# Kernel optimization log

Hardware: AMD Instinct MI355X
Metric: run time of the kernel (lower is better)

## Reference

```python
import jax, jax.numpy as jnp
import numpy as np

TOP_K = 2


def layer_norm(x, g, b, eps=1e-5):
    m = jnp.mean(x, axis=-1, keepdims=True)
    v = jnp.mean((x - m) ** 2, axis=-1, keepdims=True)
    return (x - m) * jax.lax.rsqrt(v + eps) * g + b


def setup_inputs() -> dict:
    key = jax.random.key(0)
    ks = jax.random.split(key, 6)
    B, P, D, E, K = 8, 1024, 1024, 8, TOP_K
    x = jax.random.normal(ks[0], (B, P, D), dtype=jnp.float32)
    noise = jax.random.normal(ks[1], (B * P * K, D), dtype=jnp.float32) * 1e-5
    Wg = jax.random.normal(ks[2], (D, E), dtype=jnp.float32) * 0.02
    bg = jnp.zeros((E,), dtype=jnp.float32)
    W1 = jax.random.normal(ks[3], (E, D, D), dtype=jnp.float32) * 0.02
    b1 = jnp.zeros((E, D), dtype=jnp.float32)
    W2 = jax.random.normal(ks[4], (E, D, D), dtype=jnp.float32) * 0.02
    b2 = jnp.zeros((E, D), dtype=jnp.float32)
    ln_g = jnp.ones((E, D), dtype=jnp.float32)
    ln_b = jnp.zeros((E, D), dtype=jnp.float32)
    gn_g = jnp.ones((D,), dtype=jnp.float32)
    gn_b = jnp.zeros((D,), dtype=jnp.float32)
    return {"x": x, "noise": noise, "Wg": Wg, "bg": bg, "W1": W1, "b1": b1,
            "W2": W2, "b2": b2, "ln_g": ln_g, "ln_b": ln_b, "gn_g": gn_g, "gn_b": gn_b}


def reference(x, noise, Wg, bg, W1, b1, W2, b2, ln_g, ln_b, gn_g, gn_b):
    # Eval-mode forward of Allocator (aux_loss == 0, not returned).
    B, P, D = x.shape
    E = Wg.shape[1]
    K = TOP_K
    N = B * P
    logits = jnp.einsum('bpd,de->bpe', x, Wg) + bg          # [B,P,E]
    probs = jax.nn.softmax(logits, axis=-1).reshape(N, E)
    _topk_probs, topk_idx = jax.lax.top_k(probs, K)          # probs unused in eval combine
    flat_idx = topk_idx.reshape(-1)                          # [N*K]
    sample_idx = jnp.repeat(jnp.arange(N), K)                # [N*K]
    batch_idx = sample_idx // P                              # [N*K]
    xg = x.reshape(N, D)[sample_idx] + noise                 # [N*K, D] gathered token copies
    sums = []
    for e in range(E):  # fixed small expert loop
        h = jax.nn.gelu(xg @ W1[e] + b1[e], approximate=False)
        y = h @ W2[e] + b2[e] + xg                           # Mlp + residual
        y = layer_norm(y, ln_g[e], ln_b[e])                  # Expert.norm
        m = (flat_idx == e)[:, None]
        # one_hot(batch_idx).T @ masked_output == per-batch segment sum (unweighted)
        sums.append(jax.ops.segment_sum(jnp.where(m, y, 0.0), batch_idx, num_segments=B))
    out = jnp.stack(sums, axis=0).transpose(1, 0, 2)         # [B, E, D]
    return layer_norm(out, gn_g, gn_b)
```

## Files before the change

kernel.cpp:

```cpp
#include <hip/hip_runtime.h>
#include <hip/hip_bf16.h>
#include <math.h>

#define D 1024
#define NTOK 8192
#define NSLOT 16384
#define NGRP 64
#define MAXTILE 136

typedef short bf16x8 __attribute__((ext_vector_type(8)));
typedef float floatx4 __attribute__((ext_vector_type(4)));

__device__ __forceinline__ unsigned short f2bf(float f) {
    __hip_bfloat16 h = __float2bfloat16(f);
    return *reinterpret_cast<unsigned short*>(&h);
}
__device__ __forceinline__ float bf2f(unsigned short u) {
    unsigned int v = ((unsigned int)u) << 16;
    return __uint_as_float(v);
}

__device__ __forceinline__ void load_lds16(const void* g, void* l) {
    __builtin_amdgcn_global_load_lds(
        (const __attribute__((address_space(1))) unsigned int*)g,
        (__attribute__((address_space(3))) unsigned int*)l, 16, 0, 0);
}

__global__ void zero_kernel(int* __restrict__ grp_cnt, float* __restrict__ S) {
    int i = blockIdx.x * 256 + threadIdx.x;
    if (i < NGRP) grp_cnt[i] = 0;
    if (i < 64 * D) S[i] = 0.f;
}

__global__ void route_kernel(const float* __restrict__ x, const float* __restrict__ Wg,
                             const float* __restrict__ bg, int* __restrict__ slot_e,
                             int* __restrict__ grp_cnt) {
    int wave = threadIdx.x >> 6;
    int lane = threadIdx.x & 63;
    int tok = blockIdx.x * 4 + wave;
    const float* xr = x + (size_t)tok * D;
    float acc[8] = {0.f,0.f,0.f,0.f,0.f,0.f,0.f,0.f};
    for (int k = lane; k < D; k += 64) {
        float xv = xr[k];
        const float4* w4 = reinterpret_cast<const float4*>(Wg + k * 8);
        float4 a = w4[0], b = w4[1];
        acc[0] += xv * a.x; acc[1] += xv * a.y; acc[2] += xv * a.z; acc[3] += xv * a.w;
        acc[4] += xv * b.x; acc[5] += xv * b.y; acc[6] += xv * b.z; acc[7] += xv * b.w;
    }
#pragma unroll
    for (int e = 0; e < 8; e++) {
#pragma unroll
        for (int off = 32; off > 0; off >>= 1)
            acc[e] += __shfl_xor(acc[e], off, 64);
    }
    if (lane == 0) {
        float lg[8];
#pragma unroll
        for (int e = 0; e < 8; e++) lg[e] = acc[e] + bg[e];
        int e1 = 0; float b1v = lg[0];
#pragma unroll
        for (int e = 1; e < 8; e++) if (lg[e] > b1v) { b1v = lg[e]; e1 = e; }
        int e2 = -1; float b2v = -3.0e38f;
#pragma unroll
        for (int e = 0; e < 8; e++) { if (e == e1) continue; if (lg[e] > b2v) { b2v = lg[e]; e2 = e; } }
        int b = tok >> 10;
        slot_e[2 * tok] = e1;
        slot_e[2 * tok + 1] = e2;
        atomicAdd(&grp_cnt[e1 * 8 + b], 1);
        atomicAdd(&grp_cnt[e2 * 8 + b], 1);
    }
}

__global__ void prefix_kernel(const int* __restrict__ grp_cnt, int* __restrict__ goff,
                              int* __restrict__ cursor, int2* __restrict__ tile_tab) {
    if (threadIdx.x != 0) return;
    int s = 0;
    for (int g = 0; g < NGRP; g++) { goff[g] = s; cursor[g] = s; s += grp_cnt[g]; }
    goff[NGRP] = s;
    int t = 0;
    for (int e = 0; e < 8; e++) {
        int cnt = goff[e * 8 + 8] - goff[e * 8];
        for (int m0 = 0; m0 < cnt; m0 += 128) tile_tab[t++] = make_int2(e, m0);
    }
    for (; t < MAXTILE; t++) tile_tab[t] = make_int2(-1, 0);
}

__global__ void build_xg_kernel(const float* __restrict__ x, const float* __restrict__ noise,
                                const int* __restrict__ slot_e, int* __restrict__ cursor,
                                unsigned short* __restrict__ xg) {
    int wave = threadIdx.x >> 6;
    int lane = threadIdx.x & 63;
    int slot = blockIdx.x * 4 + wave;
    int e = slot_e[slot];
    int b = slot >> 11;
    int row = 0;
    if (lane == 0) row = atomicAdd(&cursor[e * 8 + b], 1);
    row = __shfl(row, 0, 64);
    int tok = slot >> 1;
    const float4* xr = reinterpret_cast<const float4*>(x + (size_t)tok * D);
    const float4* nr = reinterpret_cast<const float4*>(noise + (size_t)slot * D);
    ushort4* og = reinterpret_cast<ushort4*>(xg + (size_t)row * D);
    for (int i = lane; i < D / 4; i += 64) {
        float4 a = xr[i], n = nr[i];
        ushort4 o;
        o.x = f2bf(a.x + n.x); o.y = f2bf(a.y + n.y);
        o.z = f2bf(a.z + n.z); o.w = f2bf(a.w + n.w);
        og[i] = o;
    }
}

__global__ void wconv_kernel(const float* __restrict__ W1, const float* __restrict__ W2,
                             unsigned short* __restrict__ W1t, unsigned short* __restrict__ W2t) {
    int z = blockIdx.y;
    int mat = z & 1, e = z >> 1;
    int kb = blockIdx.x;
    const float* src = (mat ? W2 : W1) + (size_t)e * D * D + (size_t)kb * 8 * D;
    unsigned short* dst = (mat ? W2t : W1t) + (size_t)e * D * D + (size_t)kb * (D * 8);
    int t = threadIdx.x;
    float4 v[8];
#pragma unroll
    for (int k = 0; k < 8; k++)
        v[k] = reinterpret_cast<const float4*>(src + (size_t)k * D)[t];
    const float* vf = reinterpret_cast<const float*>(v);
#pragma unroll
    for (int c = 0; c < 4; c++) {
        unsigned int w[4];
#pragma unroll
        for (int j = 0; j < 4; j++) {
            unsigned short lo = f2bf(vf[(2 * j) * 4 + c]);
            unsigned short hi = f2bf(vf[(2 * j + 1) * 4 + c]);
            w[j] = (unsigned int)lo | ((unsigned int)hi << 16);
        }
        *reinterpret_cast<uint4*>(dst + (size_t)(t * 4 + c) * 8) = make_uint4(w[0], w[1], w[2], w[3]);
    }
}

template <int MODE>
__global__ __launch_bounds__(256)
void gemm_kernel(const unsigned short* __restrict__ A,
                 const unsigned short* __restrict__ Wt,
                 const float* __restrict__ bias,
                 const unsigned short* __restrict__ xg,
                 const int2* __restrict__ tile_tab,
                 const int* __restrict__ goff,
                 unsigned short* __restrict__ Hout) {
    __shared__ unsigned short As[2][128 * 32];
    __shared__ unsigned short Bs[2][64 * 32];

    int id = blockIdx.x;
    int xcd = id & 7;
    int rem = id >> 3;
    int ntile = rem & 15;
    int t = xcd + 8 * (rem >> 4);
    int2 tt = tile_tab[t];
    int e = tt.x;
    if (e < 0) return;
    int m0 = tt.y;
    int rowBase = goff[e * 8];
    int cnt = goff[e * 8 + 8] - rowBase;
    int n0 = ntile * 64;

    int tid = threadIdx.x;
    int lane = tid & 63, wave = tid >> 6;
    int wm = wave >> 1, wn = wave & 1;
    int lr = lane & 15, quad = lane >> 4;
    int l2 = lane >> 2, l4 = lane & 3;

    int arow0 = min(m0 + (wave * 2 + 0) * 16 + l2, cnt - 1);
    int arow1 = min(m0 + (wave * 2 + 1) * 16 + l2, cnt - 1);
    const unsigned short* ap0 = A + ((size_t)(rowBase + arow0) << 10) + l4 * 8;
    const unsigned short* ap1 = A + ((size_t)(rowBase + arow1) << 10) + l4 * 8;
    const unsigned short* bp = Wt + (size_t)e * D * D
                               + (size_t)l4 * (D * 8)
                               + (size_t)(n0 + wave * 16 + l2) * 8;

    unsigned short* a_dst0[2] = { &As[0][(wave * 2 + 0) * 512 + lane * 8],
                                  &As[1][(wave * 2 + 0) * 512 + lane * 8] };
    unsigned short* a_dst1[2] = { &As[0][(wave * 2 + 1) * 512 + lane * 8],
                                  &As[1][(wave * 2 + 1) * 512 + lane * 8] };
    unsigned short* b_dst[2]  = { &Bs[0][wave * 512 + lane * 8],
                                  &Bs[1][wave * 512 + lane * 8] };

    const unsigned short* a_frag = &As[0][(wm * 64 + lr) * 32 + quad * 8];
    const unsigned short* b_frag = &Bs[0][(wn * 32 + lr) * 32 + quad * 8];

    floatx4 acc[4][2] = {};

    load_lds16(ap0, a_dst0[0]); load_lds16(ap1, a_dst1[0]); load_lds16(bp, b_dst[0]);
    ap0 += 32; ap1 += 32; bp += 4 * D * 8;

#pragma unroll 1
    for (int k0 = 0; k0 < D; k0 += 64) {
        __syncthreads();
        if (k0 + 32 < D) {
            load_lds16(ap0, a_dst0[1]); load_lds16(ap1, a_dst1[1]); load_lds16(bp, b_dst[1]);
            ap0 += 32; ap1 += 32; bp += 4 * D * 8;
        }
        {
            bf16x8 af[4], bfr[2];
#pragma unroll
            for (int i = 0; i < 4; i++)
                af[i] = *reinterpret_cast<const bf16x8*>(a_frag + i * 512);
#pragma unroll
            for (int j = 0; j < 2; j++)
                bfr[j] = *reinterpret_cast<const bf16x8*>(b_frag + j * 512);
#pragma unroll
            for (int i = 0; i < 4; i++)
#pragma unroll
                for (int j = 0; j < 2; j++)
                    acc[i][j] = __builtin_amdgcn_mfma_f32_16x16x32_bf16(af[i], bfr[j], acc[i][j], 0, 0, 0);
        }
        __syncthreads();
        if (k0 + 64 < D) {
            load_lds16(ap0, a_dst0[0]); load_lds16(ap1, a_dst1[0]); load_lds16(bp, b_dst[0]);
            ap0 += 32; ap1 += 32; bp += 4 * D * 8;
        }
        {
            bf16x8 af[4], bfr[2];
#pragma unroll
            for (int i = 0; i < 4; i++)
                af[i] = *reinterpret_cast<const bf16x8*>(a_frag + 4096 + i * 512);
#pragma unroll
            for (int j = 0; j < 2; j++)
                bfr[j] = *reinterpret_cast<const bf16x8*>(b_frag + 2048 + j * 512);
#pragma unroll
            for (int i = 0; i < 4; i++)
#pragma unroll
                for (int j = 0; j < 2; j++)
                    acc[i][j] = __builtin_amdgcn_mfma_f32_16x16x32_bf16(af[i], bfr[j], acc[i][j], 0, 0, 0);
        }
    }

#pragma unroll
    for (int i = 0; i < 4; i++) {
        int rowb = m0 + wm * 64 + i * 16 + quad * 4;
#pragma unroll
        for (int j = 0; j < 2; j++) {
            int col = n0 + wn * 32 + j * 16 + lr;
            float bia = bias[e * D + col];
#pragma unroll
            for (int r = 0; r < 4; r++) {
                int rr = rowb + r;
                if (rr < cnt) {
                    float v = acc[i][j][r] + bia;
                    size_t idx = (size_t)(rowBase + rr) * D + col;
                    if (MODE == 0) {
                        float g = 0.5f * v * (1.0f + erff(v * 0.70710678118654752f));
                        Hout[idx] = f2bf(g);
                    } else {
                        v += bf2f(xg[idx]);
                        Hout[idx] = f2bf(v);
                    }
                }
            }
        }
    }
}

__global__ void lnsum_kernel(const unsigned short* __restrict__ ybf,
                             const int* __restrict__ goff, float* __restrict__ S) {
    int grp = blockIdx.x, chunk = blockIdx.y;
    int r0 = goff[grp] + chunk * 64;
    int r1 = min(goff[grp + 1], r0 + 64);
    if (r0 >= r1) return;
    __shared__ float part[D];
    for (int i = threadIdx.x; i < D; i += 256) part[i] = 0.f;
    __syncthreads();

    int wave = threadIdx.x >> 6, lane = threadIdx.x & 63;
    float p[16] = {0.f};
    for (int r = r0 + wave; r < r1; r += 4) {
        const unsigned short* row = ybf + ((size_t)r << 10);
        float v[16];
        float s = 0.f, sq = 0.f;
#pragma unroll
        for (int c = 0; c < 4; c++) {
            ushort4 u = *reinterpret_cast<const ushort4*>(row + c * 256 + lane * 4);
            float a = bf2f(u.x), b = bf2f(u.y), cc = bf2f(u.z), d = bf2f(u.w);
            v[c * 4 + 0] = a; v[c * 4 + 1] = b; v[c * 4 + 2] = cc; v[c * 4 + 3] = d;
            s += a + b + cc + d;
            sq += a * a + b * b + cc * cc + d * d;
        }
#pragma unroll
        for (int off = 32; off > 0; off >>= 1) {
            s += __shfl_xor(s, off, 64);
            sq += __shfl_xor(sq, off, 64);
        }
        float m = s * (1.f / 1024.f);
        float rs = rsqrtf(sq * (1.f / 1024.f) - m * m + 1e-5f);
#pragma unroll
        for (int c = 0; c < 16; c++) p[c] += (v[c] - m) * rs;
    }
#pragma unroll
    for (int c = 0; c < 4; c++)
#pragma unroll
        for (int q = 0; q < 4; q++)
            atomicAdd(&part[c * 256 + lane * 4 + q], p[c * 4 + q]);
    __syncthreads();

    int e = grp >> 3, b = grp & 7;
    float* Sp = S + (size_t)(b * 8 + e) * D;
    for (int i = threadIdx.x; i < D; i += 256)
        atomicAdd(&Sp[i], part[i]);
}

__global__ void finalize_kernel(const float* __restrict__ S, const int* __restrict__ goff,
                                const float* __restrict__ ln_g, const float* __restrict__ ln_b,
                                const float* __restrict__ gn_g, const float* __restrict__ gn_b,
                                float* __restrict__ out) {
    int be = blockIdx.x;
    int b = be >> 3, e = be & 7;
    int grp = e * 8 + b;
    float cnt = (float)(goff[grp + 1] - goff[grp]);
    int tid = threadIdx.x;
    __shared__ float red[8];
    float val[4];
    float s = 0.f, sq = 0.f;
#pragma unroll
    for (int c = 0; c < 4; c++) {
        int d = tid * 4 + c;
        float v = S[(size_t)be * D + d] * ln_g[e * D + d] + cnt * ln_b[e * D + d];
        val[c] = v; s += v; sq += v * v;
    }
#pragma unroll
    for (int off = 32; off > 0; off >>= 1) {
        s += __shfl_xor(s, off, 64);
        sq += __shfl_xor(sq, off, 64);
    }
    int wave = tid >> 6, lane = tid & 63;
    if (lane == 0) { red[wave] = s; red[4 + wave] = sq; }
    __syncthreads();
    float ts = red[0] + red[1] + red[2] + red[3];
    float tq = red[4] + red[5] + red[6] + red[7];
    float m = ts / 1024.f;
    float var = tq / 1024.f - m * m;
    float rstd = rsqrtf(var + 1e-5f);
#pragma unroll
    for (int c = 0; c < 4; c++) {
        int d = tid * 4 + c;
        out[(size_t)be * D + d] = (val[c] - m) * rstd * gn_g[d] + gn_b[d];
    }
}

extern "C" void kernel_launch(void* const* d_in, const int* in_sizes, int n_in,
                              void* d_out, int out_size, void* d_ws, size_t ws_size,
                              hipStream_t stream) {
    const float* x     = (const float*)d_in[0];
    const float* noise = (const float*)d_in[1];
    const float* Wg    = (const float*)d_in[2];
    const float* bg    = (const float*)d_in[3];
    const float* W1    = (const float*)d_in[4];
    const float* b1    = (const float*)d_in[5];
    const float* W2    = (const float*)d_in[6];
    const float* b2    = (const float*)d_in[7];
    const float* ln_g  = (const float*)d_in[8];
    const float* ln_b  = (const float*)d_in[9];
    const float* gn_g  = (const float*)d_in[10];
    const float* gn_b  = (const float*)d_in[11];
    float* out = (float*)d_out;

    char* ws = (char*)d_ws;
    size_t off = 0;
    unsigned short* xg   = (unsigned short*)(ws + off); off += (size_t)NSLOT * D * 2;
    unsigned short* hb   = (unsigned short*)(ws + off); off += (size_t)NSLOT * D * 2;
    unsigned short* ybf  = (unsigned short*)(ws + off); off += (size_t)NSLOT * D * 2;
    unsigned short* W1t  = (unsigned short*)(ws + off); off += (size_t)8 * D * D * 2;
    unsigned short* W2t  = (unsigned short*)(ws + off); off += (size_t)8 * D * D * 2;
    int* slot_e          = (int*)(ws + off);            off += (size_t)NSLOT * 4;
    int* grp_cnt         = (int*)(ws + off);            off += 256;
    int* goff            = (int*)(ws + off);            off += 512;
    int* cursor          = (int*)(ws + off);            off += 256;
    int2* tile_tab       = (int2*)(ws + off);           off += MAXTILE * 8;
    float* S             = (float*)(ws + off);          off += (size_t)64 * D * 4;

    zero_kernel<<<256, 256, 0, stream>>>(grp_cnt, S);
    route_kernel<<<NTOK / 4, 256, 0, stream>>>(x, Wg, bg, slot_e, grp_cnt);
    prefix_kernel<<<1, 64, 0, stream>>>(grp_cnt, goff, cursor, tile_tab);
    wconv_kernel<<<dim3(128, 16), 256, 0, stream>>>(W1, W2, W1t, W2t);
    build_xg_kernel<<<NSLOT / 4, 256, 0, stream>>>(x, noise, slot_e, cursor, xg);
    gemm_kernel<0><<<dim3(2176), 256, 0, stream>>>(xg, W1t, b1, xg, tile_tab, goff, hb);
    gemm_kernel<1><<<dim3(2176), 256, 0, stream>>>(hb, W2t, b2, xg, tile_tab, goff, ybf);
    lnsum_kernel<<<dim3(64, 32), 256, 0, stream>>>(ybf, goff, S);
    finalize_kernel<<<64, 256, 0, stream>>>(S, goff, ln_g, ln_b, gn_g, gn_b, out);
}
```

Baseline: 538.6 us.

## Widen GEMM tiles to 128x128, parallelize prefix scan, simplify weight conversion

The expert GEMM block tile grows from 128x64 to 128x128, so each wave holds a 4x4 set of MFMA accumulators and the grid is halved, which raises operand reuse per LDS load. The single-thread prefix kernel becomes a 64-lane shuffle scan with parallel tile-table fill. The weight conversion now reads coalesced scalars per column instead of float4 rows, and lnsum processes 128 rows per block. The trade-off is higher register and LDS use in the GEMM, which may lower occupancy, plus fewer blocks for the grouped tiles.

Measured after the change: 564.7 us. +4.8%, slower.

```diff
diff --git a/kernel.cpp b/kernel.cpp
--- a/kernel.cpp
+++ b/kernel.cpp
@@ -73,16 +73,34 @@
 
 __global__ void prefix_kernel(const int* __restrict__ grp_cnt, int* __restrict__ goff,
                               int* __restrict__ cursor, int2* __restrict__ tile_tab) {
-    if (threadIdx.x != 0) return;
-    int s = 0;
-    for (int g = 0; g < NGRP; g++) { goff[g] = s; cursor[g] = s; s += grp_cnt[g]; }
-    goff[NGRP] = s;
-    int t = 0;
-    for (int e = 0; e < 8; e++) {
-        int cnt = goff[e * 8 + 8] - goff[e * 8];
-        for (int m0 = 0; m0 < cnt; m0 += 128) tile_tab[t++] = make_int2(e, m0);
-    }
-    for (; t < MAXTILE; t++) tile_tab[t] = make_int2(-1, 0);
+    __shared__ int g[65];
+    __shared__ int tstart[9];
+    int lane = threadIdx.x;
+    int c = grp_cnt[lane];
+    int s = c;
+#pragma unroll
+    for (int off = 1; off < 64; off <<= 1) {
+        int v = __shfl_up(s, off, 64);
+        if (lane >= off) s += v;
+    }
+    int excl = s - c;
+    goff[lane] = excl; cursor[lane] = excl; g[lane] = excl;
+    if (lane == 63) { goff[64] = s; g[64] = s; }
+    __syncthreads();
+    if (lane == 0) {
+        int t = 0;
+#pragma unroll
+        for (int e = 0; e < 8; e++) { tstart[e] = t; t += (g[8 * e + 8] - g[8 * e] + 127) >> 7; }
+        tstart[8] = t;
+    }
+    __syncthreads();
+    for (int t = lane; t < MAXTILE; t += 64) {
+        int e = -1, m0 = 0;
+#pragma unroll
+        for (int k = 0; k < 8; k++)
+            if (t >= tstart[k] && t < tstart[k + 1]) { e = k; m0 = (t - tstart[k]) << 7; }
+        tile_tab[t] = make_int2(e, m0);
+    }
 }
 
 __global__ void build_xg_kernel(const float* __restrict__ x, const float* __restrict__ noise,
@@ -117,21 +135,17 @@
     const float* src = (mat ? W2 : W1) + (size_t)e * D * D + (size_t)kb * 8 * D;
     unsigned short* dst = (mat ? W2t : W1t) + (size_t)e * D * D + (size_t)kb * (D * 8);
     int t = threadIdx.x;
-    float4 v[8];
-#pragma unroll
-    for (int k = 0; k < 8; k++)
-        v[k] = reinterpret_cast<const float4*>(src + (size_t)k * D)[t];
-    const float* vf = reinterpret_cast<const float*>(v);
 #pragma unroll
     for (int c = 0; c < 4; c++) {
+        int n = c * 256 + t;
         unsigned int w[4];
 #pragma unroll
         for (int j = 0; j < 4; j++) {
-            unsigned short lo = f2bf(vf[(2 * j) * 4 + c]);
-            unsigned short hi = f2bf(vf[(2 * j + 1) * 4 + c]);
+            unsigned short lo = f2bf(src[(size_t)(2 * j) * D + n]);
+            unsigned short hi = f2bf(src[(size_t)(2 * j + 1) * D + n]);
             w[j] = (unsigned int)lo | ((unsigned int)hi << 16);
         }
-        *reinterpret_cast<uint4*>(dst + (size_t)(t * 4 + c) * 8) = make_uint4(w[0], w[1], w[2], w[3]);
+        *reinterpret_cast<uint4*>(dst + (size_t)n * 8) = make_uint4(w[0], w[1], w[2], w[3]);
     }
 }
 
@@ -145,20 +159,21 @@
                  const int* __restrict__ goff,
                  unsigned short* __restrict__ Hout) {
     __shared__ unsigned short As[2][128 * 32];
-    __shared__ unsigned short Bs[2][64 * 32];
+    __shared__ unsigned short Bs[2][128 * 32];
 
     int id = blockIdx.x;
     int xcd = id & 7;
     int rem = id >> 3;
-    int ntile = rem & 15;
-    int t = xcd + 8 * (rem >> 4);
-    int2 tt = tile_tab[t];
+    int ntile = rem & 7;
+    int mseq = rem >> 3;
+    int2 tt = tile_tab[xcd + 8 * mseq];
     int e = tt.x;
     if (e < 0) return;
     int m0 = tt.y;
     int rowBase = goff[e * 8];
     int cnt = goff[e * 8 + 8] - rowBase;
-    int n0 = ntile * 64;
+    if (m0 >= cnt) return;
+    int n0 = ntile * 128;
 
     int tid = threadIdx.x;
     int lane = tid & 63, wave = tid >> 6;
@@ -170,63 +185,68 @@
     int arow1 = min(m0 + (wave * 2 + 1) * 16 + l2, cnt - 1);
     const unsigned short* ap0 = A + ((size_t)(rowBase + arow0) << 10) + l4 * 8;
     const unsigned short* ap1 = A + ((size_t)(rowBase + arow1) << 10) + l4 * 8;
-    const unsigned short* bp = Wt + (size_t)e * D * D
-                               + (size_t)l4 * (D * 8)
-                               + (size_t)(n0 + wave * 16 + l2) * 8;
-
-    unsigned short* a_dst0[2] = { &As[0][(wave * 2 + 0) * 512 + lane * 8],
-                                  &As[1][(wave * 2 + 0) * 512 + lane * 8] };
-    unsigned short* a_dst1[2] = { &As[0][(wave * 2 + 1) * 512 + lane * 8],
-                                  &As[1][(wave * 2 + 1) * 512 + lane * 8] };
-    unsigned short* b_dst[2]  = { &Bs[0][wave * 512 + lane * 8],
-                                  &Bs[1][wave * 512 + lane * 8] };
+    const unsigned short* wb = Wt + ((size_t)e << 20) + (size_t)l4 * 8192;
+    const unsigned short* bp0 = wb + (size_t)(n0 + (wave * 2 + 0) * 16 + l2) * 8;
+    const unsigned short* bp1 = wb + (size_t)(n0 + (wave * 2 + 1) * 16 + l2) * 8;
+
+    unsigned short* ad0[2] = { &As[0][(wave * 2 + 0) * 512 + lane * 8],
+                               &As[1][(wave * 2 + 0) * 512 + lane * 8] };
+    unsigned short* ad1[2] = { &As[0][(wave * 2 + 1) * 512 + lane * 8],
+                               &As[1][(wave * 2 + 1) * 512 + lane * 8] };
+    unsigned short* bd0[2] = { &Bs[0][(wave * 2 + 0) * 512 + lane * 8],
+                               &Bs[1][(wave * 2 + 0) * 512 + lane * 8] };
+    unsigned short* bd1[2] = { &Bs[0][(wave * 2 + 1) * 512 + lane * 8],
+                               &Bs[1][(wave * 2 + 1) * 512 + lane * 8] };
 
     const unsigned short* a_frag = &As[0][(wm * 64 + lr) * 32 + quad * 8];
-    const unsigned short* b_frag = &Bs[0][(wn * 32 + lr) * 32 + quad * 8];
-
-    floatx4 acc[4][2] = {};
-
-    load_lds16(ap0, a_dst0[0]); load_lds16(ap1, a_dst1[0]); load_lds16(bp, b_dst[0]);
-    ap0 += 32; ap1 += 32; bp += 4 * D * 8;
+    const unsigned short* b_frag = &Bs[0][(wn * 64 + lr) * 32 + quad * 8];
+
+    floatx4 acc[4][4] = {};
+
+    load_lds16(ap0, ad0[0]); load_lds16(ap1, ad1[0]);
+    load_lds16(bp0, bd0[0]); load_lds16(bp1, bd1[0]);
+    ap0 += 32; ap1 += 32; bp0 += 32768; bp1 += 32768;
 
 #pragma unroll 1
     for (int k0 = 0; k0 < D; k0 += 64) {
         __syncthreads();
         if (k0 + 32 < D) {
-            load_lds16(ap0, a_dst0[1]); load_lds16(ap1, a_dst1[1]); load_lds16(bp, b_dst[1]);
-            ap0 += 32; ap1 += 32; bp += 4 * D * 8;
+            load_lds16(ap0, ad0[1]); load_lds16(ap1, ad1[1]);
+            load_lds16(bp0, bd0[1]); load_lds16(bp1, bd1[1]);
+            ap0 += 32; ap1 += 32; bp0 += 32768; bp1 += 32768;
         }
         {
-            bf16x8 af[4], bfr[2];
+            bf16x8 af[4], bfr[4];
 #pragma unroll
             for (int i = 0; i < 4; i++)
                 af[i] = *reinterpret_cast<const bf16x8*>(a_frag + i * 512);
 #pragma unroll
-            for (int j = 0; j < 2; j++)
+            for (int j = 0; j < 4; j++)
                 bfr[j] = *reinterpret_cast<const bf16x8*>(b_frag + j * 512);
 #pragma unroll
             for (int i = 0; i < 4; i++)
 #pragma unroll
-                for (int j = 0; j < 2; j++)
+                for (int j = 0; j < 4; j++)
                     acc[i][j] = __builtin_amdgcn_mfma_f32_16x16x32_bf16(af[i], bfr[j], acc[i][j], 0, 0, 0);
         }
         __syncthreads();
         if (k0 + 64 < D) {
-            load_lds16(ap0, a_dst0[0]); load_lds16(ap1, a_dst1[0]); load_lds16(bp, b_dst[0]);
-            ap0 += 32; ap1 += 32; bp += 4 * D * 8;
+            load_lds16(ap0, ad0[0]); load_lds16(ap1, ad1[0]);
+            load_lds16(bp0, bd0[0]); load_lds16(bp1, bd1[0]);
+            ap0 += 32; ap1 += 32; bp0 += 32768; bp1 += 32768;
         }
         {
-            bf16x8 af[4], bfr[2];
+            bf16x8 af[4], bfr[4];
 #pragma unroll
             for (int i = 0; i < 4; i++)
                 af[i] = *reinterpret_cast<const bf16x8*>(a_frag + 4096 + i * 512);
 #pragma unroll
-            for (int j = 0; j < 2; j++)
-                bfr[j] = *reinterpret_cast<const bf16x8*>(b_frag + 2048 + j * 512);
+            for (int j = 0; j < 4; j++)
+                bfr[j] = *reinterpret_cast<const bf16x8*>(b_frag + 4096 + j * 512);
 #pragma unroll
             for (int i = 0; i < 4; i++)
 #pragma unroll
-                for (int j = 0; j < 2; j++)
+                for (int j = 0; j < 4; j++)
                     acc[i][j] = __builtin_amdgcn_mfma_f32_16x16x32_bf16(af[i], bfr[j], acc[i][j], 0, 0, 0);
         }
     }
@@ -235,15 +255,15 @@
     for (int i = 0; i < 4; i++) {
         int rowb = m0 + wm * 64 + i * 16 + quad * 4;
 #pragma unroll
-        for (int j = 0; j < 2; j++) {
-            int col = n0 + wn * 32 + j * 16 + lr;
+        for (int j = 0; j < 4; j++) {
+            int col = n0 + wn * 64 + j * 16 + lr;
             float bia = bias[e * D + col];
 #pragma unroll
             for (int r = 0; r < 4; r++) {
                 int rr = rowb + r;
                 if (rr < cnt) {
                     float v = acc[i][j][r] + bia;
-                    size_t idx = (size_t)(rowBase + rr) * D + col;
+                    size_t idx = (((size_t)(rowBase + rr)) << 10) + col;
                     if (MODE == 0) {
                         float g = 0.5f * v * (1.0f + erff(v * 0.70710678118654752f));
                         Hout[idx] = f2bf(g);
@@ -260,8 +280,8 @@
 __global__ void lnsum_kernel(const unsigned short* __restrict__ ybf,
                              const int* __restrict__ goff, float* __restrict__ S) {
     int grp = blockIdx.x, chunk = blockIdx.y;
-    int r0 = goff[grp] + chunk * 64;
-    int r1 = min(goff[grp + 1], r0 + 64);
+    int r0 = goff[grp] + chunk * 128;
+    int r1 = min(goff[grp + 1], r0 + 128);
     if (r0 >= r1) return;
     __shared__ float part[D];
     for (int i = threadIdx.x; i < D; i += 256) part[i] = 0.f;
@@ -378,8 +398,8 @@
     prefix_kernel<<<1, 64, 0, stream>>>(grp_cnt, goff, cursor, tile_tab);
     wconv_kernel<<<dim3(128, 16), 256, 0, stream>>>(W1, W2, W1t, W2t);
     build_xg_kernel<<<NSLOT / 4, 256, 0, stream>>>(x, noise, slot_e, cursor, xg);
-    gemm_kernel<0><<<dim3(2176), 256, 0, stream>>>(xg, W1t, b1, xg, tile_tab, goff, hb);
-    gemm_kernel<1><<<dim3(2176), 256, 0, stream>>>(hb, W2t, b2, xg, tile_tab, goff, ybf);
-    lnsum_kernel<<<dim3(64, 32), 256, 0, stream>>>(ybf, goff, S);
+    gemm_kernel<0><<<dim3(1088), 256, 0, stream>>>(xg, W1t, b1, xg, tile_tab, goff, hb);
+    gemm_kernel<1><<<dim3(1088), 256, 0, stream>>>(hb, W2t, b2, xg, tile_tab, goff, ybf);
+    lnsum_kernel<<<dim3(64, 16), 256, 0, stream>>>(ybf, goff, S);
     finalize_kernel<<<64, 256, 0, stream>>>(S, goff, ln_g, ln_b, gn_g, gn_b, out);
 }
```
